# Optimization experiments

Hardware: AMD Instinct MI355X
Metric: run time of the kernel (lower is better)

The kernel has to match this reference:

```python
import jax, jax.numpy as jnp
import numpy as np

T, H, E, I, K = 4096, 1024, 8, 1024, 2  # tokens, hidden, experts, intermediate, top_k


def setup_inputs() -> dict:
    key = jax.random.key(0)
    k1, k2, k3, k4, k5 = jax.random.split(key, 5)
    x = jax.random.normal(k1, (T, H), dtype=jnp.float32)
    router_logits = jax.random.normal(k2, (T, E), dtype=jnp.float32)
    per_expert_scale = jnp.ones((E,), dtype=jnp.float32)
    # FusedMoE layout: w13 = fused [gate; up] projection [E, 2I, H], w2 = down [E, H, I]
    w13 = jax.random.normal(k3, (E, 2 * I, H), dtype=jnp.float32) * 0.02
    w2 = jax.random.normal(k4, (E, H, I), dtype=jnp.float32) * 0.02
    return {"x": x, "router_logits": router_logits,
            "per_expert_scale": per_expert_scale, "w13": w13, "w2": w2}


def reference(x, router_logits, per_expert_scale, w13, w2):
    # --- Gemma4 routing: softmax over ALL experts -> top-k -> renormalize ---
    _, topk_ids = jax.lax.top_k(router_logits, K)              # [T, K] int32
    probs = jax.nn.softmax(router_logits, axis=-1)             # [T, E]
    indicator = jax.nn.one_hot(topk_ids, E, dtype=probs.dtype).sum(axis=-2)  # [T, E]
    gate = indicator * probs
    renorm = gate.sum(axis=-1, keepdims=True)
    renorm = jnp.where(renorm > 0.0, renorm, 1.0)
    dispatch = gate / renorm                                   # zero off top-k
    # per_expert_scale folded into routing weights (only top-k slots nonzero)
    combine_w = dispatch * per_expert_scale[None, :]           # [T, E]

    # --- expert FFN (gelu gate * up -> down), combined with routing weights ---
    w1, w3 = w13[:, :I, :], w13[:, I:, :]                      # [E, I, H] each
    g = jnp.einsum('th,eih->tei', x, w1)                       # gate proj
    u = jnp.einsum('th,eih->tei', x, w3)                       # up proj
    h = jax.nn.gelu(g, approximate=False) * u                  # exact GELU (torch default)
    y = jnp.einsum('tei,ehi->teh', h, w2)                      # down proj
    out = jnp.einsum('te,teh->th', combine_w, y)               # weighted combine
    return out
```

## Files before the change

kernel.cpp:

```cpp
#include <hip/hip_runtime.h>
#include <hip/hip_bf16.h>

#define T_TOK 4096
#define H_DIM 1024
#define E_NUM 8
#define I_DIM 1024
#define PAD_CAP 9216
#define RBLK 16

typedef __attribute__((ext_vector_type(4))) float f32x4;
typedef __attribute__((ext_vector_type(8))) short bf16x8;

__device__ __forceinline__ unsigned short f2b(float f) {
  union { float f; unsigned int u; } v; v.f = f;
  unsigned int r = v.u + 0x7fffu + ((v.u >> 16) & 1u);
  return (unsigned short)(r >> 16);
}

__device__ __forceinline__ void async_copy16(const void* g, void* l) {
  __builtin_amdgcn_global_load_lds(
      (const __attribute__((address_space(1))) void*)g,
      (__attribute__((address_space(3))) void*)l, 16, 0, 0);
}

__global__ __launch_bounds__(256) void k_prep(
    const float* __restrict__ x, const float* __restrict__ logits,
    const float* __restrict__ scale,
    const float* __restrict__ w13, const float* __restrict__ w2,
    unsigned short* __restrict__ xb, unsigned short* __restrict__ w13b,
    unsigned short* __restrict__ w2b,
    int* __restrict__ tids, float* __restrict__ cw, int* __restrict__ cnt) {
  const int b = blockIdx.x;
  if (b < RBLK) {
    __shared__ int s_cnt[E_NUM];
    const int tid = threadIdx.x;
    if (tid < E_NUM) s_cnt[tid] = 0;
    __syncthreads();
    int t = b * 256 + tid;
    float l[E_NUM];
    *(float4*)(l)     = *(const float4*)(logits + (size_t)t * E_NUM);
    *(float4*)(l + 4) = *(const float4*)(logits + (size_t)t * E_NUM + 4);
    float m = l[0];
#pragma unroll
    for (int i = 1; i < E_NUM; ++i) m = fmaxf(m, l[i]);
    float p[E_NUM]; float s = 0.f;
#pragma unroll
    for (int i = 0; i < E_NUM; ++i) { p[i] = expf(l[i] - m); s += p[i]; }
    int i0 = 0; float b0 = l[0];
#pragma unroll
    for (int i = 1; i < E_NUM; ++i) if (l[i] > b0) { b0 = l[i]; i0 = i; }
    int i1 = -1; float b1 = -1e30f;
#pragma unroll
    for (int i = 0; i < E_NUM; ++i) if (i != i0 && l[i] > b1) { b1 = l[i]; i1 = i; }
    float g0 = p[i0] / s, g1 = p[i1] / s;
    float r = g0 + g1;
    cw[t * 2]     = g0 / r * scale[i0];
    cw[t * 2 + 1] = g1 / r * scale[i1];
    tids[t * 2] = i0; tids[t * 2 + 1] = i1;
    atomicAdd(&s_cnt[i0], 1);
    atomicAdd(&s_cnt[i1], 1);
    __syncthreads();
    if (tid < E_NUM) cnt[b * E_NUM + tid] = s_cnt[tid];
    return;
  }
  const int cb = b - RBLK;
  const float* src; unsigned short* dst; size_t base;
  if (cb < 2048)       { src = x;   dst = xb;   base = (size_t)cb * 2048; }
  else if (cb < 10240) { src = w13; dst = w13b; base = (size_t)(cb - 2048) * 2048; }
  else                 { src = w2;  dst = w2b;  base = (size_t)(cb - 10240) * 2048; }
  size_t i = base + (size_t)threadIdx.x * 8;
  float4 f0 = *(const float4*)(src + i);
  float4 f1 = *(const float4*)(src + i + 4);
  uint4 pk;
  pk.x = (unsigned)f2b(f0.x) | ((unsigned)f2b(f0.y) << 16);
  pk.y = (unsigned)f2b(f0.z) | ((unsigned)f2b(f0.w) << 16);
  pk.z = (unsigned)f2b(f1.x) | ((unsigned)f2b(f1.y) << 16);
  pk.w = (unsigned)f2b(f1.z) | ((unsigned)f2b(f1.w) << 16);
  *(uint4*)(dst + i) = pk;
}

__global__ __launch_bounds__(256) void k_scatter(
    const int* __restrict__ tids, const int* __restrict__ cnt,
    int* __restrict__ pad_off, int* __restrict__ perm, int* __restrict__ inv) {
  __shared__ int s_cnt[RBLK * E_NUM];
  __shared__ int s_tot[E_NUM];
  __shared__ int s_off[E_NUM];
  __shared__ int s_base[E_NUM];
  __shared__ int l_cnt[E_NUM];
  const int b = blockIdx.x, tid = threadIdx.x;
  if (tid < RBLK * E_NUM) s_cnt[tid] = cnt[tid];
  if (tid < E_NUM) l_cnt[tid] = 0;
  __syncthreads();
  if (tid < E_NUM) {
    int tot = 0;
#pragma unroll
    for (int bb = 0; bb < RBLK; ++bb) tot += s_cnt[bb * E_NUM + tid];
    s_tot[tid] = tot;
  }
  __syncthreads();
  if (tid < E_NUM) {
    int off = 0;
    for (int e = 0; e < tid; ++e) off += (s_tot[e] + 127) & ~127;
    s_off[tid] = off;
    int myb = off;
    for (int bb = 0; bb < b; ++bb) myb += s_cnt[bb * E_NUM + tid];
    s_base[tid] = myb;
    if (b == 0) {
      pad_off[tid] = off;
      if (tid == E_NUM - 1) pad_off[E_NUM] = off + ((s_tot[tid] + 127) & ~127);
    }
  }
  __syncthreads();
  if (b < E_NUM) {
    int start = s_off[b] + s_tot[b];
    int end   = s_off[b] + ((s_tot[b] + 127) & ~127);
    for (int i = start + tid; i < end; i += 256) perm[i] = -1;
  }
  int t = b * 256 + tid;
  int i0 = tids[t * 2], i1 = tids[t * 2 + 1];
  int r0 = atomicAdd(&l_cnt[i0], 1);
  int s0 = s_base[i0] + r0;
  perm[s0] = t * 2; inv[t * 2] = s0;
  int r1 = atomicAdd(&l_cnt[i1], 1);
  int s1 = s_base[i1] + r1;
  perm[s1] = t * 2 + 1; inv[t * 2 + 1] = s1;
}

__global__ __launch_bounds__(256, 2) void k_gemm1(
    const unsigned short* __restrict__ xbf,
    const unsigned short* __restrict__ w13b,
    const int* __restrict__ perm, const int* __restrict__ pad_off,
    unsigned short* __restrict__ h_buf) {
  __shared__ __align__(16) unsigned short a_lds[128 * 64];
  __shared__ __align__(16) unsigned short b_lds[128 * 64];
  const int tid = threadIdx.x;
  const int wave = tid >> 6, lane = tid & 63;
  const int row0 = blockIdx.y * 128;
  if (row0 >= pad_off[E_NUM]) return;
  int e = 0;
#pragma unroll
  for (int i = 1; i < E_NUM; ++i) if (row0 >= pad_off[i]) e = i;
  const int iBase = blockIdx.x * 64;

  const int srcChunk = (lane & 7) ^ ((lane >> 3) & 7);

  const unsigned short* agbase[4];
#pragma unroll
  for (int j = 0; j < 4; ++j) {
    int r = j * 32 + wave * 8 + (lane >> 3);
    int p = perm[row0 + r];
    int tok = (p < 0) ? 0 : (p >> 1);
    agbase[j] = xbf + (size_t)tok * H_DIM + srcChunk * 8;
  }
  const unsigned short* bgbase[4];
#pragma unroll
  for (int j = 0; j < 4; ++j) {
    int brow = j * 32 + wave * 8 + (lane >> 3);
    int seg = brow >> 5, half = seg & 1;
    int col = iBase + (seg >> 1) * 32 + (brow & 31);
    bgbase[j] = w13b + ((size_t)e * 2 * I_DIM + half * I_DIM + col) * H_DIM + srcChunk * 8;
  }

  f32x4 acc[4][4];
#pragma unroll
  for (int mi = 0; mi < 4; ++mi)
#pragma unroll
    for (int ni = 0; ni < 4; ++ni) acc[mi][ni] = (f32x4)(0.f);

  const int wm = wave >> 1, wn = wave & 1;
  const int ml = lane & 15, quad = lane >> 4;

  for (int k0 = 0; k0 < H_DIM; k0 += 64) {
    __syncthreads();
#pragma unroll
    for (int j = 0; j < 4; ++j)
      async_copy16(agbase[j] + k0, a_lds + (j * 256 + wave * 64) * 8);
#pragma unroll
    for (int j = 0; j < 4; ++j)
      async_copy16(bgbase[j] + k0, b_lds + (j * 256 + wave * 64) * 8);
    __syncthreads();
#pragma unroll
    for (int ks = 0; ks < 2; ++ks) {
      const int ch = ((ks * 4 + quad) ^ (ml & 7)) * 8;
      bf16x8 af[4], bfr[4];
#pragma unroll
      for (int mi = 0; mi < 4; ++mi)
        af[mi] = *(const bf16x8*)(a_lds + (wm * 64 + mi * 16 + ml) * 64 + ch);
#pragma unroll
      for (int ni = 0; ni < 4; ++ni)
        bfr[ni] = *(const bf16x8*)(b_lds + (wn * 64 + ni * 16 + ml) * 64 + ch);
#pragma unroll
      for (int mi = 0; mi < 4; ++mi)
#pragma unroll
        for (int ni = 0; ni < 4; ++ni)
          acc[mi][ni] = __builtin_amdgcn_mfma_f32_16x16x32_bf16(af[mi], bfr[ni], acc[mi][ni], 0, 0, 0);
    }
  }
#pragma unroll
  for (int mi = 0; mi < 4; ++mi) {
#pragma unroll
    for (int nc = 0; nc < 2; ++nc) {
      f32x4 g = acc[mi][nc];
      f32x4 uu = acc[mi][nc + 2];
#pragma unroll
      for (int r = 0; r < 4; ++r) {
        int row = row0 + wm * 64 + mi * 16 + quad * 4 + r;
        int col = iBase + wn * 32 + nc * 16 + ml;
        float gg = g[r];
        float q  = gg * (2.3022080f + 0.10294324f * gg * gg);
        float z  = __builtin_amdgcn_exp2f(-q);
        float hv = gg * uu[r] * __builtin_amdgcn_rcpf(1.f + z);
        h_buf[(size_t)row * I_DIM + col] = f2b(hv);
      }
    }
  }
}

__global__ __launch_bounds__(256, 2) void k_gemm2(
    const unsigned short* __restrict__ h_buf,
    const unsigned short* __restrict__ w2b,
    const int* __restrict__ pad_off,
    unsigned short* __restrict__ y) {
  __shared__ __align__(16) unsigned short a_lds[128 * 64];
  __shared__ __align__(16) unsigned short b_lds[64 * 64];
  const int tid = threadIdx.x;
  const int wave = tid >> 6, lane = tid & 63;
  const int row0 = blockIdx.y * 128;
  if (row0 >= pad_off[E_NUM]) return;
  int e = 0;
#pragma unroll
  for (int i = 1; i < E_NUM; ++i) if (row0 >= pad_off[i]) e = i;
  const int cBase = blockIdx.x * 64;
  const int srcChunk = (lane & 7) ^ ((lane >> 3) & 7);

  const unsigned short* agbase[4];
#pragma unroll
  for (int j = 0; j < 4; ++j) {
    int r = j * 32 + wave * 8 + (lane >> 3);
    agbase[j] = h_buf + (size_t)(row0 + r) * I_DIM + srcChunk * 8;
  }
  const unsigned short* bgbase[2];
#pragma unroll
  for (int j = 0; j < 2; ++j) {
    int brow = j * 32 + wave * 8 + (lane >> 3);
    bgbase[j] = w2b + ((size_t)e * H_DIM + cBase + brow) * I_DIM + srcChunk * 8;
  }
  f32x4 acc[2][4];
#pragma unroll
  for (int mi = 0; mi < 2; ++mi)
#pragma unroll
    for (int ni = 0; ni < 4; ++ni) acc[mi][ni] = (f32x4)(0.f);
  const int ml = lane & 15, quad = lane >> 4;

  for (int k0 = 0; k0 < I_DIM; k0 += 64) {
    __syncthreads();
#pragma unroll
    for (int j = 0; j < 4; ++j)
      async_copy16(agbase[j] + k0, a_lds + (j * 256 + wave * 64) * 8);
#pragma unroll
    for (int j = 0; j < 2; ++j)
      async_copy16(bgbase[j] + k0, b_lds + (j * 256 + wave * 64) * 8);
    __syncthreads();
#pragma unroll
    for (int ks = 0; ks < 2; ++ks) {
      const int ch = ((ks * 4 + quad) ^ (ml & 7)) * 8;
      bf16x8 af[2], bfr[4];
#pragma unroll
      for (int mi = 0; mi < 2; ++mi)
        af[mi] = *(const bf16x8*)(a_lds + (wave * 32 + mi * 16 + ml) * 64 + ch);
#pragma unroll
      for (int ni = 0; ni < 4; ++ni)
        bfr[ni] = *(const bf16x8*)(b_lds + (ni * 16 + ml) * 64 + ch);
#pragma unroll
      for (int mi = 0; mi < 2; ++mi)
#pragma unroll
        for (int ni = 0; ni < 4; ++ni)
          acc[mi][ni] = __builtin_amdgcn_mfma_f32_16x16x32_bf16(af[mi], bfr[ni], acc[mi][ni], 0, 0, 0);
    }
  }
#pragma unroll
  for (int mi = 0; mi < 2; ++mi) {
#pragma unroll
    for (int ni = 0; ni < 4; ++ni) {
#pragma unroll
      for (int r = 0; r < 4; ++r) {
        int row = row0 + wave * 32 + mi * 16 + quad * 4 + r;
        int col = cBase + ni * 16 + ml;
        y[(size_t)row * H_DIM + col] = f2b(acc[mi][ni][r]);
      }
    }
  }
}

__global__ void k_combine(const unsigned short* __restrict__ y,
                          const int* __restrict__ inv, const float* __restrict__ cw,
                          float* __restrict__ out) {
  const int t = blockIdx.x;
  const int c = threadIdx.x * 4;
  int s0 = inv[t * 2], s1 = inv[t * 2 + 1];
  float c0 = cw[t * 2], c1 = cw[t * 2 + 1];
  uint2 a = *(const uint2*)(y + (size_t)s0 * H_DIM + c);
  uint2 b = *(const uint2*)(y + (size_t)s1 * H_DIM + c);
  union { unsigned v; float f; } w;
  float4 o;
  float alo, ahi, blo, bhi;
  w.v = a.x << 16;          alo = w.f;
  w.v = a.x & 0xffff0000u;  ahi = w.f;
  w.v = b.x << 16;          blo = w.f;
  w.v = b.x & 0xffff0000u;  bhi = w.f;
  o.x = c0 * alo + c1 * blo;
  o.y = c0 * ahi + c1 * bhi;
  w.v = a.y << 16;          alo = w.f;
  w.v = a.y & 0xffff0000u;  ahi = w.f;
  w.v = b.y << 16;          blo = w.f;
  w.v = b.y & 0xffff0000u;  bhi = w.f;
  o.z = c0 * alo + c1 * blo;
  o.w = c0 * ahi + c1 * bhi;
  *(float4*)(out + (size_t)t * H_DIM + c) = o;
}

extern "C" void kernel_launch(void* const* d_in, const int* in_sizes, int n_in,
                              void* d_out, int out_size, void* d_ws, size_t ws_size,
                              hipStream_t stream) {
  const float* x      = (const float*)d_in[0];
  const float* logits = (const float*)d_in[1];
  const float* scale  = (const float*)d_in[2];
  const float* w13    = (const float*)d_in[3];
  const float* w2     = (const float*)d_in[4];
  float* out = (float*)d_out;

  char* ws = (char*)d_ws;
  int*   pad_off = (int*)(ws + 128);
  int*   cnt     = (int*)(ws + 1024);
  int*   tids    = (int*)(ws + 4096);
  float* cw      = (float*)(ws + 65536);
  int*   perm    = (int*)(ws + 131072);
  int*   inv     = (int*)(ws + 196608);
  unsigned short* xb    = (unsigned short*)(ws + 0x40000);
  unsigned short* h_buf = (unsigned short*)(ws + 0x900000);
  unsigned short* w13b  = (unsigned short*)(ws + 0x1C00000);
  unsigned short* ybuf  = w13b;
  unsigned short* w2b   = (unsigned short*)(ws + 0x3C00000);

  k_prep<<<14336 + RBLK, 256, 0, stream>>>(x, logits, scale, w13, w2,
                                           xb, w13b, w2b, tids, cw, cnt);
  k_scatter<<<RBLK, 256, 0, stream>>>(tids, cnt, pad_off, perm, inv);
  k_gemm1<<<dim3(16, PAD_CAP / 128), 256, 0, stream>>>(xb, w13b, perm, pad_off, h_buf);
  k_gemm2<<<dim3(16, PAD_CAP / 128), 256, 0, stream>>>(h_buf, w2b, pad_off, ybuf);
  k_combine<<<T_TOK, 256, 0, stream>>>(ybuf, inv, cw, out);
}
```

Measured before the change: 242.2 us.

## Overlap w2 bf16 conversion with gemm1 and enlarge gemm2 tile to 128x128

The fp32-to-bf16 conversion of w2 moves out of the prep kernel and into extra blocks appended to the gemm1 grid, so it can run alongside the gate/up GEMM instead of serially before it. Separately, gemm2 now uses 128x128 output tiles with a 2x2 wave layout, which doubles reuse of the A tile from LDS and halves the number of column blocks. The bigger tile raises accumulator register pressure, and launch bounds of 3 blocks per SM may force spills. The extra gemm1 blocks also compete with the GEMM tiles for CUs.

```diff
diff --git a/kernel.cpp b/kernel.cpp
--- a/kernel.cpp
+++ b/kernel.cpp
@@ -7,6 +7,7 @@
 #define I_DIM 1024
 #define PAD_CAP 9216
 #define RBLK 16
+#define G1_ROWBLK (PAD_CAP / 128)
 
 typedef __attribute__((ext_vector_type(4))) float f32x4;
 typedef __attribute__((ext_vector_type(8))) short bf16x8;
@@ -23,51 +24,9 @@
       (__attribute__((address_space(3))) void*)l, 16, 0, 0);
 }
 
-__global__ __launch_bounds__(256) void k_prep(
-    const float* __restrict__ x, const float* __restrict__ logits,
-    const float* __restrict__ scale,
-    const float* __restrict__ w13, const float* __restrict__ w2,
-    unsigned short* __restrict__ xb, unsigned short* __restrict__ w13b,
-    unsigned short* __restrict__ w2b,
-    int* __restrict__ tids, float* __restrict__ cw, int* __restrict__ cnt) {
-  const int b = blockIdx.x;
-  if (b < RBLK) {
-    __shared__ int s_cnt[E_NUM];
-    const int tid = threadIdx.x;
-    if (tid < E_NUM) s_cnt[tid] = 0;
-    __syncthreads();
-    int t = b * 256 + tid;
-    float l[E_NUM];
-    *(float4*)(l)     = *(const float4*)(logits + (size_t)t * E_NUM);
-    *(float4*)(l + 4) = *(const float4*)(logits + (size_t)t * E_NUM + 4);
-    float m = l[0];
-#pragma unroll
-    for (int i = 1; i < E_NUM; ++i) m = fmaxf(m, l[i]);
-    float p[E_NUM]; float s = 0.f;
-#pragma unroll
-    for (int i = 0; i < E_NUM; ++i) { p[i] = expf(l[i] - m); s += p[i]; }
-    int i0 = 0; float b0 = l[0];
-#pragma unroll
-    for (int i = 1; i < E_NUM; ++i) if (l[i] > b0) { b0 = l[i]; i0 = i; }
-    int i1 = -1; float b1 = -1e30f;
-#pragma unroll
-    for (int i = 0; i < E_NUM; ++i) if (i != i0 && l[i] > b1) { b1 = l[i]; i1 = i; }
-    float g0 = p[i0] / s, g1 = p[i1] / s;
-    float r = g0 + g1;
-    cw[t * 2]     = g0 / r * scale[i0];
-    cw[t * 2 + 1] = g1 / r * scale[i1];
-    tids[t * 2] = i0; tids[t * 2 + 1] = i1;
-    atomicAdd(&s_cnt[i0], 1);
-    atomicAdd(&s_cnt[i1], 1);
-    __syncthreads();
-    if (tid < E_NUM) cnt[b * E_NUM + tid] = s_cnt[tid];
-    return;
-  }
-  const int cb = b - RBLK;
-  const float* src; unsigned short* dst; size_t base;
-  if (cb < 2048)       { src = x;   dst = xb;   base = (size_t)cb * 2048; }
-  else if (cb < 10240) { src = w13; dst = w13b; base = (size_t)(cb - 2048) * 2048; }
-  else                 { src = w2;  dst = w2b;  base = (size_t)(cb - 10240) * 2048; }
+__device__ __forceinline__ void conv_chunk(const float* __restrict__ src,
+                                           unsigned short* __restrict__ dst,
+                                           size_t base) {
   size_t i = base + (size_t)threadIdx.x * 8;
   float4 f0 = *(const float4*)(src + i);
   float4 f1 = *(const float4*)(src + i + 4);
@@ -77,6 +36,49 @@
   pk.z = (unsigned)f2b(f1.x) | ((unsigned)f2b(f1.y) << 16);
   pk.w = (unsigned)f2b(f1.z) | ((unsigned)f2b(f1.w) << 16);
   *(uint4*)(dst + i) = pk;
+}
+
+__global__ __launch_bounds__(256) void k_prep(
+    const float* __restrict__ x, const float* __restrict__ logits,
+    const float* __restrict__ scale, const float* __restrict__ w13,
+    unsigned short* __restrict__ xb, unsigned short* __restrict__ w13b,
+    int* __restrict__ tids, float* __restrict__ cw, int* __restrict__ cnt) {
+  const int b = blockIdx.x;
+  if (b < RBLK) {
+    __shared__ int s_cnt[E_NUM];
+    const int tid = threadIdx.x;
+    if (tid < E_NUM) s_cnt[tid] = 0;
+    __syncthreads();
+    int t = b * 256 + tid;
+    float l[E_NUM];
+    *(float4*)(l)     = *(const float4*)(logits + (size_t)t * E_NUM);
+    *(float4*)(l + 4) = *(const float4*)(logits + (size_t)t * E_NUM + 4);
+    float m = l[0];
+#pragma unroll
+    for (int i = 1; i < E_NUM; ++i) m = fmaxf(m, l[i]);
+    float p[E_NUM]; float s = 0.f;
+#pragma unroll
+    for (int i = 0; i < E_NUM; ++i) { p[i] = expf(l[i] - m); s += p[i]; }
+    int i0 = 0; float b0 = l[0];
+#pragma unroll
+    for (int i = 1; i < E_NUM; ++i) if (l[i] > b0) { b0 = l[i]; i0 = i; }
+    int i1 = -1; float b1 = -1e30f;
+#pragma unroll
+    for (int i = 0; i < E_NUM; ++i) if (i != i0 && l[i] > b1) { b1 = l[i]; i1 = i; }
+    float g0 = p[i0] / s, g1 = p[i1] / s;
+    float r = g0 + g1;
+    cw[t * 2]     = g0 / r * scale[i0];
+    cw[t * 2 + 1] = g1 / r * scale[i1];
+    tids[t * 2] = i0; tids[t * 2 + 1] = i1;
+    atomicAdd(&s_cnt[i0], 1);
+    atomicAdd(&s_cnt[i1], 1);
+    __syncthreads();
+    if (tid < E_NUM) cnt[b * E_NUM + tid] = s_cnt[tid];
+    return;
+  }
+  const int cb = b - RBLK;
+  if (cb < 2048) conv_chunk(x,   xb,   (size_t)cb * 2048);
+  else           conv_chunk(w13, w13b, (size_t)(cb - 2048) * 2048);
 }
 
 __global__ __launch_bounds__(256) void k_scatter(
@@ -130,12 +132,19 @@
     const unsigned short* __restrict__ xbf,
     const unsigned short* __restrict__ w13b,
     const int* __restrict__ perm, const int* __restrict__ pad_off,
-    unsigned short* __restrict__ h_buf) {
+    unsigned short* __restrict__ h_buf,
+    const float* __restrict__ w2, unsigned short* __restrict__ w2b) {
   __shared__ __align__(16) unsigned short a_lds[128 * 64];
   __shared__ __align__(16) unsigned short b_lds[128 * 64];
+  const int by = blockIdx.y;
+  if (by >= G1_ROWBLK) {
+    int cb = (by - G1_ROWBLK) * 16 + blockIdx.x;
+    conv_chunk(w2, w2b, (size_t)cb * 2048);
+    return;
+  }
   const int tid = threadIdx.x;
   const int wave = tid >> 6, lane = tid & 63;
-  const int row0 = blockIdx.y * 128;
+  const int row0 = by * 128;
   if (row0 >= pad_off[E_NUM]) return;
   int e = 0;
 #pragma unroll
@@ -216,13 +225,13 @@
   }
 }
 
-__global__ __launch_bounds__(256, 2) void k_gemm2(
+__global__ __launch_bounds__(256, 3) void k_gemm2(
     const unsigned short* __restrict__ h_buf,
     const unsigned short* __restrict__ w2b,
     const int* __restrict__ pad_off,
     unsigned short* __restrict__ y) {
   __shared__ __align__(16) unsigned short a_lds[128 * 64];
-  __shared__ __align__(16) unsigned short b_lds[64 * 64];
+  __shared__ __align__(16) unsigned short b_lds[128 * 64];
   const int tid = threadIdx.x;
   const int wave = tid >> 6, lane = tid & 63;
   const int row0 = blockIdx.y * 128;
@@ -230,7 +239,7 @@
   int e = 0;
 #pragma unroll
   for (int i = 1; i < E_NUM; ++i) if (row0 >= pad_off[i]) e = i;
-  const int cBase = blockIdx.x * 64;
+  const int cBase = blockIdx.x * 128;
   const int srcChunk = (lane & 7) ^ ((lane >> 3) & 7);
 
   const unsigned short* agbase[4];
@@ -239,17 +248,19 @@
     int r = j * 32 + wave * 8 + (lane >> 3);
     agbase[j] = h_buf + (size_t)(row0 + r) * I_DIM + srcChunk * 8;
   }
-  const unsigned short* bgbase[2];
-#pragma unroll
-  for (int j = 0; j < 2; ++j) {
+  const unsigned short* bgbase[4];
+#pragma unroll
+  for (int j = 0; j < 4; ++j) {
     int brow = j * 32 + wave * 8 + (lane >> 3);
     bgbase[j] = w2b + ((size_t)e * H_DIM + cBase + brow) * I_DIM + srcChunk * 8;
   }
-  f32x4 acc[2][4];
-#pragma unroll
-  for (int mi = 0; mi < 2; ++mi)
+  f32x4 acc[4][4];
+#pragma unroll
+  for (int mi = 0; mi < 4; ++mi)
 #pragma unroll
     for (int ni = 0; ni < 4; ++ni) acc[mi][ni] = (f32x4)(0.f);
+
+  const int wm = wave >> 1, wn = wave & 1;
   const int ml = lane & 15, quad = lane >> 4;
 
   for (int k0 = 0; k0 < I_DIM; k0 += 64) {
@@ -258,34 +269,34 @@
     for (int j = 0; j < 4; ++j)
       async_copy16(agbase[j] + k0, a_lds + (j * 256 + wave * 64) * 8);
 #pragma unroll
-    for (int j = 0; j < 2; ++j)
+    for (int j = 0; j < 4; ++j)
       async_copy16(bgbase[j] + k0, b_lds + (j * 256 + wave * 64) * 8);
     __syncthreads();
 #pragma unroll
     for (int ks = 0; ks < 2; ++ks) {
       const int ch = ((ks * 4 + quad) ^ (ml & 7)) * 8;
-      bf16x8 af[2], bfr[4];
-#pragma unroll
-      for (int mi = 0; mi < 2; ++mi)
-        af[mi] = *(const bf16x8*)(a_lds + (wave * 32 + mi * 16 + ml) * 64 + ch);
+      bf16x8 af[4], bfr[4];
+#pragma unroll
+      for (int mi = 0; mi < 4; ++mi)
+        af[mi] = *(const bf16x8*)(a_lds + (wm * 64 + mi * 16 + ml) * 64 + ch);
 #pragma unroll
       for (int ni = 0; ni < 4; ++ni)
-        bfr[ni] = *(const bf16x8*)(b_lds + (ni * 16 + ml) * 64 + ch);
-#pragma unroll
-      for (int mi = 0; mi < 2; ++mi)
+        bfr[ni] = *(const bf16x8*)(b_lds + (wn * 64 + ni * 16 + ml) * 64 + ch);
+#pragma unroll
+      for (int mi = 0; mi < 4; ++mi)
 #pragma unroll
         for (int ni = 0; ni < 4; ++ni)
           acc[mi][ni] = __builtin_amdgcn_mfma_f32_16x16x32_bf16(af[mi], bfr[ni], acc[mi][ni], 0, 0, 0);
     }
   }
 #pragma unroll
-  for (int mi = 0; mi < 2; ++mi) {
+  for (int mi = 0; mi < 4; ++mi) {
 #pragma unroll
     for (int ni = 0; ni < 4; ++ni) {
 #pragma unroll
       for (int r = 0; r < 4; ++r) {
-        int row = row0 + wave * 32 + mi * 16 + quad * 4 + r;
-        int col = cBase + ni * 16 + ml;
+        int row = row0 + wm * 64 + mi * 16 + quad * 4 + r;
+        int col = cBase + wn * 64 + ni * 16 + ml;
         y[(size_t)row * H_DIM + col] = f2b(acc[mi][ni][r]);
       }
     }
@@ -342,10 +353,11 @@
   unsigned short* ybuf  = w13b;
   unsigned short* w2b   = (unsigned short*)(ws + 0x3C00000);
 
-  k_prep<<<14336 + RBLK, 256, 0, stream>>>(x, logits, scale, w13, w2,
-                                           xb, w13b, w2b, tids, cw, cnt);
+  k_prep<<<10240 + RBLK, 256, 0, stream>>>(x, logits, scale, w13,
+                                           xb, w13b, tids, cw, cnt);
   k_scatter<<<RBLK, 256, 0, stream>>>(tids, cnt, pad_off, perm, inv);
-  k_gemm1<<<dim3(16, PAD_CAP / 128), 256, 0, stream>>>(xb, w13b, perm, pad_off, h_buf);
-  k_gemm2<<<dim3(16, PAD_CAP / 128), 256, 0, stream>>>(h_buf, w2b, pad_off, ybuf);
+  k_gemm1<<<dim3(16, G1_ROWBLK + 256), 256, 0, stream>>>(xb, w13b, perm, pad_off,
+                                                         h_buf, w2, w2b);
+  k_gemm2<<<dim3(8, PAD_CAP / 128), 256, 0, stream>>>(h_buf, w2b, pad_off, ybuf);
   k_combine<<<T_TOK, 256, 0, stream>>>(ybuf, inv, cw, out);
 }
```

Measured after the change: 225.4 us. 7.0% less time.
